# Performance work log

Hardware: AMD Instinct MI355X
Metric: run time of the kernel (lower is better)

## Reference

```python
import jax, jax.numpy as jnp
import numpy as np

DIM = 192
HEADS = 6
WS = (4, 8, 8)  # window size (D, H, W)
N = WS[0] * WS[1] * WS[2]  # 256 tokens per window
NW = 64
B_ = 256  # batch * nW


def _relative_position_index(ws):
    d, h, w = ws
    coords = jnp.stack(jnp.meshgrid(jnp.arange(d), jnp.arange(h), jnp.arange(w), indexing='ij'))
    coords = coords.reshape(3, -1)  # (3, N)
    rel = coords[:, :, None] - coords[:, None, :]  # (3, N, N)
    rel = rel.transpose(1, 2, 0) + jnp.array([d - 1, h - 1, w - 1])
    idx = rel[..., 0] * ((2 * h - 1) * (2 * w - 1)) + rel[..., 1] * (2 * w - 1) + rel[..., 2]
    return idx.astype(jnp.int32)  # (N, N)


def setup_inputs() -> dict:
    key = jax.random.key(0)
    ks = jax.random.split(key, 7)
    table_rows = (2 * WS[0] - 1) * (2 * WS[1] - 1) * (2 * WS[2] - 1)  # 1575
    return {
        'x': jax.random.normal(ks[0], (B_, N, DIM), dtype=jnp.float32),
        'mask': jax.random.normal(ks[1], (NW, N, N), dtype=jnp.float32),
        'qkv_w': jax.random.normal(ks[2], (DIM, 3 * DIM), dtype=jnp.float32) * 0.02,
        'qkv_b': jnp.zeros((3 * DIM,), dtype=jnp.float32),
        'proj_w': jax.random.normal(ks[3], (DIM, DIM), dtype=jnp.float32) * 0.02,
        'proj_b': jnp.zeros((DIM,), dtype=jnp.float32),
        'bias_table': jax.random.normal(ks[4], (table_rows, HEADS), dtype=jnp.float32) * 0.02,
        'rel_index': _relative_position_index(WS),
    }


def reference(x, mask, qkv_w, qkv_b, proj_w, proj_b, bias_table, rel_index):
    B, Ntok, C = x.shape
    hd = C // HEADS
    scale = hd ** (-0.5)
    qkv = (x @ qkv_w + qkv_b).reshape(B, Ntok, 3, HEADS, hd)
    qkv = qkv.transpose(2, 0, 3, 1, 4)  # (3, B, H, N, hd)
    q, k, v = qkv[0], qkv[1], qkv[2]
    attn = jnp.einsum('bhnd,bhmd->bhnm', q * scale, k)  # (B, H, N, N)
    # gathered relative-position bias: (N, N, H) -> (H, N, N)
    bias = bias_table[rel_index.reshape(-1)].reshape(Ntok, Ntok, HEADS).transpose(2, 0, 1)
    attn = attn + bias[None]
    nW = mask.shape[0]
    attn = attn.reshape(B // nW, nW, HEADS, Ntok, Ntok) + mask[None, :, None]
    attn = attn.reshape(B, HEADS, Ntok, Ntok)
    attn = jax.nn.softmax(attn, axis=-1)
    out = jnp.einsum('bhnm,bhmd->bhnd', attn, v)  # (B, H, N, hd)
    out = out.transpose(0, 2, 1, 3).reshape(B, Ntok, C)
    out = out @ proj_w + proj_b
    return out
```

## Files before the change

### kernel.cpp

```cpp
#include <hip/hip_runtime.h>
#include <cstdint>
#include <math.h>

#define DIMC 192
#define NTOK 256
#define HEADS 6
#define HD 32
#define L2E 1.4426950408889634f

typedef __bf16 bf16x8 __attribute__((ext_vector_type(8)));
typedef __bf16 bf16x4 __attribute__((ext_vector_type(4)));
typedef float f32x4 __attribute__((ext_vector_type(4)));

__device__ __forceinline__ void gload_lds16(const __bf16* g, __bf16* l) {
    __builtin_amdgcn_global_load_lds((const __attribute__((address_space(1))) void*)g,
                                     (__attribute__((address_space(3))) void*)l, 16, 0, 0);
}

__global__ void prep(const float* __restrict__ x, __bf16* __restrict__ xb,
                     const float* __restrict__ qkv_w, __bf16* __restrict__ wqt,
                     const float* __restrict__ proj_w, __bf16* __restrict__ wpt,
                     const float* __restrict__ table, const int* __restrict__ rel,
                     __bf16* __restrict__ biasb) {
    const int bid = blockIdx.x, t = threadIdx.x;
    if (bid < 6144) {
        int i = bid * 256 + t;
        float4 a = ((const float4*)x)[i * 2];
        float4 b = ((const float4*)x)[i * 2 + 1];
        bf16x8 o = {(__bf16)a.x, (__bf16)a.y, (__bf16)a.z, (__bf16)a.w,
                    (__bf16)b.x, (__bf16)b.y, (__bf16)b.z, (__bf16)b.w};
        ((bf16x8*)xb)[i] = o;
    } else if (bid < 6576) {
        int i = (bid - 6144) * 256 + t;
        int n = i / DIMC, k = i - n * DIMC;
        wqt[i] = (__bf16)qkv_w[(size_t)k * 576 + n];
    } else if (bid < 6720) {
        int i = (bid - 6576) * 256 + t;
        int n = i / DIMC, k = i - n * DIMC;
        wpt[i] = (__bf16)proj_w[(size_t)k * DIMC + n];
    } else {
        int i = (bid - 6720) * 256 + t;
        int h = i >> 16;
        int r = i & 65535;
        biasb[i] = (__bf16)(table[rel[r] * 6 + h] * L2E);
    }
}

__launch_bounds__(256, 2)
__global__ void qkvbm(const __bf16* __restrict__ A, const __bf16* __restrict__ Wt,
                      const float* __restrict__ bias,
                      __bf16* __restrict__ qo, __bf16* __restrict__ ko, __bf16* __restrict__ vo,
                      const float* __restrict__ mask, const __bf16* __restrict__ biasb,
                      __bf16* __restrict__ bm) {
    __shared__ __bf16 As[256 * 64];
    __shared__ __bf16 Bs[96 * 64];
    const int t = threadIdx.x;
    const int lin = blockIdx.x;

    if (lin >= 1536) {
        int i = (lin - 1536) * 256 + t;
        int w = i >> 13, oct = i & 8191;
        float4 m0 = ((const float4*)mask)[(size_t)w * 16384 + oct * 2];
        float4 m1 = ((const float4*)mask)[(size_t)w * 16384 + oct * 2 + 1];
        #pragma unroll
        for (int h = 0; h < 6; ++h) {
            bf16x8 bb = ((const bf16x8*)biasb)[h * 8192 + oct];
            bf16x8 o = {(__bf16)(m0.x * L2E + (float)bb[0]), (__bf16)(m0.y * L2E + (float)bb[1]),
                        (__bf16)(m0.z * L2E + (float)bb[2]), (__bf16)(m0.w * L2E + (float)bb[3]),
                        (__bf16)(m1.x * L2E + (float)bb[4]), (__bf16)(m1.y * L2E + (float)bb[5]),
                        (__bf16)(m1.z * L2E + (float)bb[6]), (__bf16)(m1.w * L2E + (float)bb[7])};
            ((bf16x8*)bm)[(size_t)(w * 6 + h) * 8192 + oct] = o;
        }
        return;
    }

    const int wv = t >> 6, lane = t & 63;
    const int l16 = lane & 15, quad = lane >> 4;
    const int xcd = lin & 7, pos = lin >> 3;
    const int bx = pos % 6;
    const int by = xcd + (pos / 6) * 8;
    const int m0 = by * 256;
    const int j0 = bx * 96;

    f32x4 acc[4][6];
    #pragma unroll
    for (int mt = 0; mt < 4; ++mt)
        #pragma unroll
        for (int nt = 0; nt < 6; ++nt)
            acc[mt][nt] = (f32x4){0.f, 0.f, 0.f, 0.f};

    for (int kit = 0; kit < 3; ++kit) {
        const int k0 = kit * 64;
        #pragma unroll
        for (int gi = 0; gi < 8; ++gi) {
            int g = wv * 8 + gi;
            int cid = g * 64 + lane;
            int row = cid >> 3, kcs = cid & 7;
            int kcg = kcs ^ (row & 7);
            gload_lds16(A + (size_t)(m0 + row) * DIMC + k0 + kcg * 8, As + g * 512);
        }
        #pragma unroll
        for (int gi = 0; gi < 3; ++gi) {
            int g = wv * 3 + gi;
            int cid = g * 64 + lane;
            int n = cid >> 3, kcs = cid & 7;
            int kcg = kcs ^ (n & 7);
            gload_lds16(Wt + (size_t)(j0 + n) * DIMC + k0 + kcg * 8, Bs + g * 512);
        }
        __syncthreads();
        #pragma unroll
        for (int kk = 0; kk < 2; ++kk) {
            bf16x8 af[4], bfr[6];
            #pragma unroll
            for (int mt = 0; mt < 4; ++mt) {
                int row = wv * 64 + mt * 16 + l16;
                int ch = (kk * 4 + quad) ^ (row & 7);
                af[mt] = *(const bf16x8*)(As + row * 64 + ch * 8);
            }
            #pragma unroll
            for (int nt = 0; nt < 6; ++nt) {
                int n = nt * 16 + l16;
                int ch = (kk * 4 + quad) ^ (n & 7);
                bfr[nt] = *(const bf16x8*)(Bs + n * 64 + ch * 8);
            }
            #pragma unroll
            for (int mt = 0; mt < 4; ++mt)
                #pragma unroll
                for (int nt = 0; nt < 6; ++nt)
                    acc[mt][nt] = __builtin_amdgcn_mfma_f32_16x16x32_bf16(af[mt], bfr[nt], acc[mt][nt], 0, 0, 0);
        }
        __syncthreads();
    }

    const int which = bx >> 1;
    __bf16* outp = which == 0 ? qo : (which == 1 ? ko : vo);
    const float sc = which == 0 ? (0.17677669529663687f * L2E) : 1.0f;
    float bq[6];
    #pragma unroll
    for (int nt = 0; nt < 6; ++nt) bq[nt] = bias[j0 + nt * 16 + l16];
    const int cloc = (bx & 1) * 96;
    const int b = m0 >> 8;

    if (which != 2) {
        __bf16* tile = As + wv * 4096;
        const int TP = 104;
        #pragma unroll
        for (int mt = 0; mt < 4; ++mt) {
            #pragma unroll
            for (int nt = 0; nt < 6; ++nt)
                #pragma unroll
                for (int r = 0; r < 4; ++r)
                    tile[(quad * 4 + r) * TP + nt * 16 + l16] = (__bf16)((acc[mt][nt][r] + bq[nt]) * sc);
            int row = lane >> 2;
            #pragma unroll
            for (int it = 0; it < 3; ++it) {
                int c8 = (lane & 3) + it * 4;
                bf16x8 val = *(const bf16x8*)(tile + row * TP + c8 * 8);
                int n = wv * 64 + mt * 16 + row;
                int cw = cloc + c8 * 8;
                int h = cw >> 5, d0 = cw & 31;
                *(bf16x8*)(outp + (((size_t)b * HEADS + h) * NTOK + n) * HD + d0) = val;
            }
        }
    } else {
        __bf16* tileT = As + wv * 4096;
        #pragma unroll
        for (int mt = 0; mt < 4; ++mt) {
            #pragma unroll
            for (int nt = 0; nt < 6; ++nt)
                #pragma unroll
                for (int r = 0; r < 4; ++r)
                    tileT[(nt * 16 + l16) * 16 + quad * 4 + r] = (__bf16)(acc[mt][nt][r] + bq[nt]);
            int n0 = wv * 64 + mt * 16;
            #pragma unroll
            for (int it = 0; it < 3; ++it) {
                int qid = lane + 64 * it;
                int col = qid >> 1, half = qid & 1;
                bf16x8 val = *(const bf16x8*)(tileT + col * 16 + half * 8);
                int cw = cloc + col;
                int h = cw >> 5, d = cw & 31;
                *(bf16x8*)(outp + (((size_t)b * HEADS + h) * HD + d) * NTOK + n0 + half * 8) = val;
            }
        }
    }
}

__launch_bounds__(256, 4)
__global__ void attn_mfma(const __bf16* __restrict__ qg, const __bf16* __restrict__ kg,
                          const __bf16* __restrict__ vtg, const __bf16* __restrict__ bm,
                          __bf16* __restrict__ aout) {
    __shared__ __bf16 Ps[4][16][40];
    __shared__ float  Sums[4][64];

    const int lin = blockIdx.x;
    const int xcd = lin & 7, pos = lin >> 3;
    const int g = xcd + (pos >> 2) * 8;
    const int i4 = pos & 3;
    const int h = g % 6, w = g / 6;
    const int b = i4 * 64 + w;
    const int bh = b * HEADS + h;

    const int t = threadIdx.x;
    const int wv = t >> 6, lane = t & 63;
    const int l16 = lane & 15, quad = lane >> 4;
    const int q0 = wv * 64;
    const size_t base = (size_t)bh * (NTOK * HD);

    bf16x8 qf[4];
    #pragma unroll
    for (int qt = 0; qt < 4; ++qt)
        qf[qt] = *(const bf16x8*)(qg + base + (size_t)(q0 + qt * 16 + l16) * HD + quad * 8);

    f32x4 o[4][2];
    #pragma unroll
    for (int qt = 0; qt < 4; ++qt)
        #pragma unroll
        for (int dt = 0; dt < 2; ++dt)
            o[qt][dt] = (f32x4){0.f, 0.f, 0.f, 0.f};
    float rsum[4] = {};

    const __bf16* kp  = kg  + base + (size_t)l16 * HD + quad * 8;
    const __bf16* vp  = vtg + base + (size_t)l16 * NTOK + quad * 8;
    const __bf16* bmq = bm + (size_t)(w * 6 + h) * 65536 + (size_t)(q0 + l16) * 256 + quad * 4;

    bf16x8 kf[2];
    kf[0] = *(const bf16x8*)(kp);
    kf[1] = *(const bf16x8*)(kp + 16 * HD);

    for (int c = 0; c < 8; ++c) {
        const int kb = c * 32;
        bf16x4 bmv[4][2];
        #pragma unroll
        for (int qt = 0; qt < 4; ++qt)
            #pragma unroll
            for (int kt = 0; kt < 2; ++kt)
                bmv[qt][kt] = *(const bf16x4*)(bmq + qt * 4096 + kb + kt * 16);
        bf16x8 vf[2];
        #pragma unroll
        for (int dt = 0; dt < 2; ++dt)
            vf[dt] = *(const bf16x8*)(vp + dt * 16 * NTOK + kb);
        bf16x8 kfn[2];
        if (c < 7) {
            kfn[0] = *(const bf16x8*)(kp + (kb + 32) * HD);
            kfn[1] = *(const bf16x8*)(kp + (kb + 48) * HD);
        }

        #pragma unroll
        for (int qt = 0; qt < 4; ++qt) {
            #pragma unroll
            for (int kt = 0; kt < 2; ++kt) {
                f32x4 s = (f32x4){0.f, 0.f, 0.f, 0.f};
                s = __builtin_amdgcn_mfma_f32_16x16x32_bf16(kf[kt], qf[qt], s, 0, 0, 0);
                bf16x4 pk;
                #pragma unroll
                for (int r = 0; r < 4; ++r) {
                    float p = __builtin_amdgcn_exp2f(s[r] + (float)bmv[qt][kt][r]);
                    rsum[qt] += p;
                    pk[r] = (__bf16)p;
                }
                *(bf16x4*)(&Ps[wv][l16][kt * 16 + quad * 4]) = pk;
            }
            bf16x8 pf = *(const bf16x8*)(&Ps[wv][l16][quad * 8]);
            #pragma unroll
            for (int dt = 0; dt < 2; ++dt)
                o[qt][dt] = __builtin_amdgcn_mfma_f32_16x16x32_bf16(pf, vf[dt], o[qt][dt], 0, 0, 0);
        }
        if (c < 7) { kf[0] = kfn[0]; kf[1] = kfn[1]; }
    }

    #pragma unroll
    for (int qt = 0; qt < 4; ++qt) {
        float s = rsum[qt];
        s += __shfl_xor(s, 16);
        s += __shfl_xor(s, 32);
        if (quad == 0) Sums[wv][qt * 16 + l16] = 1.0f / s;
    }
    #pragma unroll
    for (int qt = 0; qt < 4; ++qt) {
        f32x4 inv = *(const f32x4*)(&Sums[wv][qt * 16 + quad * 4]);
        #pragma unroll
        for (int dt = 0; dt < 2; ++dt)
            #pragma unroll
            for (int r = 0; r < 4; ++r) {
                int qrow = q0 + qt * 16 + quad * 4 + r;
                aout[((size_t)b * NTOK + qrow) * DIMC + h * HD + dt * 16 + l16] =
                    (__bf16)(o[qt][dt][r] * inv[r]);
            }
    }
}

__launch_bounds__(256, 2)
__global__ void proj_mfma(const __bf16* __restrict__ A, const __bf16* __restrict__ Wt,
                          const float* __restrict__ bias, float* __restrict__ out) {
    __shared__ __bf16 As[256 * 64];
    __shared__ __bf16 Bs[96 * 64];
    const int t = threadIdx.x;
    const int wv = t >> 6, lane = t & 63;
    const int l16 = lane & 15, quad = lane >> 4;

    const int lin = blockIdx.x + blockIdx.y * 2;
    const int xcd = lin & 7, pos = lin >> 3;
    const int bx = pos & 1;
    const int by = xcd + (pos >> 1) * 8;

    const int m0 = by * 256;
    const int j0 = bx * 96;

    f32x4 acc[4][6];
    #pragma unroll
    for (int mt = 0; mt < 4; ++mt)
        #pragma unroll
        for (int nt = 0; nt < 6; ++nt)
            acc[mt][nt] = (f32x4){0.f, 0.f, 0.f, 0.f};

    for (int kit = 0; kit < 3; ++kit) {
        const int k0 = kit * 64;
        #pragma unroll
        for (int gi = 0; gi < 8; ++gi) {
            int g = wv * 8 + gi;
            int cid = g * 64 + lane;
            int row = cid >> 3, kcs = cid & 7;
            int kcg = kcs ^ (row & 7);
            gload_lds16(A + (size_t)(m0 + row) * DIMC + k0 + kcg * 8, As + g * 512);
        }
        #pragma unroll
        for (int gi = 0; gi < 3; ++gi) {
            int g = wv * 3 + gi;
            int cid = g * 64 + lane;
            int n = cid >> 3, kcs = cid & 7;
            int kcg = kcs ^ (n & 7);
            gload_lds16(Wt + (size_t)(j0 + n) * DIMC + k0 + kcg * 8, Bs + g * 512);
        }
        __syncthreads();
        #pragma unroll
        for (int kk = 0; kk < 2; ++kk) {
            bf16x8 af[4], bfr[6];
            #pragma unroll
            for (int mt = 0; mt < 4; ++mt) {
                int row = wv * 64 + mt * 16 + l16;
                int ch = (kk * 4 + quad) ^ (row & 7);
                af[mt] = *(const bf16x8*)(As + row * 64 + ch * 8);
            }
            #pragma unroll
            for (int nt = 0; nt < 6; ++nt) {
                int n = nt * 16 + l16;
                int ch = (kk * 4 + quad) ^ (n & 7);
                bfr[nt] = *(const bf16x8*)(Bs + n * 64 + ch * 8);
            }
            #pragma unroll
            for (int mt = 0; mt < 4; ++mt)
                #pragma unroll
                for (int nt = 0; nt < 6; ++nt)
                    acc[mt][nt] = __builtin_amdgcn_mfma_f32_16x16x32_bf16(af[mt], bfr[nt], acc[mt][nt], 0, 0, 0);
        }
        __syncthreads();
    }

    #pragma unroll
    for (int nt = 0; nt < 6; ++nt) {
        int colg = j0 + nt * 16 + l16;
        float bv = bias[colg];
        #pragma unroll
        for (int mt = 0; mt < 4; ++mt)
            #pragma unroll
            for (int r = 0; r < 4; ++r) {
                int token = m0 + wv * 64 + mt * 16 + quad * 4 + r;
                out[(size_t)token * DIMC + colg] = acc[mt][nt][r] + bv;
            }
    }
}

extern "C" void kernel_launch(void* const* d_in, const int* in_sizes, int n_in,
                              void* d_out, int out_size, void* d_ws, size_t ws_size,
                              hipStream_t stream) {
    const float* x          = (const float*)d_in[0];
    const float* mask       = (const float*)d_in[1];
    const float* qkv_w      = (const float*)d_in[2];
    const float* qkv_b      = (const float*)d_in[3];
    const float* proj_w     = (const float*)d_in[4];
    const float* proj_b     = (const float*)d_in[5];
    const float* bias_table = (const float*)d_in[6];
    const int*   rel_index  = (const int*)d_in[7];

    char* ws = (char*)d_ws;
    __bf16* xb    = (__bf16*)(ws);
    __bf16* q     = (__bf16*)(ws + 25165824);
    __bf16* k     = (__bf16*)(ws + 50331648);
    __bf16* vT    = (__bf16*)(ws + 75497472);
    __bf16* biasb = (__bf16*)(ws + 100663296);
    __bf16* wqt   = (__bf16*)(ws + 102236160);
    __bf16* wpt   = (__bf16*)(ws + 102457344);
    __bf16* aoutb = xb;
    __bf16* bm    = (__bf16*)d_out;

    prep<<<8256, 256, 0, stream>>>(x, xb, qkv_w, wqt, proj_w, wpt, bias_table, rel_index, biasb);
    qkvbm<<<3584, 256, 0, stream>>>(xb, wqt, qkv_b, q, k, vT, mask, biasb, bm);
    attn_mfma<<<1536, 256, 0, stream>>>(q, k, vT, bm, aoutb);
    proj_mfma<<<dim3(2, 256), 256, 0, stream>>>(aoutb, wpt, proj_b, (float*)d_out);
}
```

Before: 233.2 us.

## Stage K and V^T tiles in swizzled LDS and prefetch the bias-mask one chunk ahead

The attention kernel now copies the whole K and V^T tiles for its (batch, head) pair into LDS with global_load_lds. An XOR swizzle is applied to avoid bank conflicts, and the MFMA operands are then read from LDS. Previously each of the four waves loaded them separately from global memory. The bias-plus-mask loads are double-buffered one chunk ahead, and the final normalisation broadcasts row sums with shuffles instead of an LDS scratch array. The cost is 32KB of extra LDS per block, which may lower occupancy, plus a block-wide barrier before compute begins.

```diff
diff --git a/kernel.cpp b/kernel.cpp
--- a/kernel.cpp
+++ b/kernel.cpp
@@ -189,8 +189,9 @@
 __global__ void attn_mfma(const __bf16* __restrict__ qg, const __bf16* __restrict__ kg,
                           const __bf16* __restrict__ vtg, const __bf16* __restrict__ bm,
                           __bf16* __restrict__ aout) {
+    __shared__ __bf16 Ks[NTOK * 32];
+    __shared__ __bf16 VTs[HD * 256];
     __shared__ __bf16 Ps[4][16][40];
-    __shared__ float  Sums[4][64];
 
     const int lin = blockIdx.x;
     const int xcd = lin & 7, pos = lin >> 3;
@@ -206,6 +207,24 @@
     const int q0 = wv * 64;
     const size_t base = (size_t)bh * (NTOK * HD);
 
+    #pragma unroll
+    for (int it = 0; it < 4; ++it) {
+        int grp = it * 4 + wv;
+        int cid = grp * 64 + lane;
+        int row = cid >> 2, cc = cid & 3;
+        int scc = cc ^ ((row >> 1) & 3);
+        gload_lds16(kg + base + row * HD + scc * 8, Ks + grp * 512);
+    }
+    #pragma unroll
+    for (int it = 0; it < 4; ++it) {
+        int grp = it * 4 + wv;
+        int cid = grp * 64 + lane;
+        int row = cid >> 5, cc = cid & 31;
+        int scc = cc ^ (row & 7);
+        gload_lds16(vtg + base + row * NTOK + scc * 8, VTs + grp * 512);
+    }
+    __syncthreads();
+
     bf16x8 qf[4];
     #pragma unroll
     for (int qt = 0; qt < 4; ++qt)
@@ -219,30 +238,36 @@
             o[qt][dt] = (f32x4){0.f, 0.f, 0.f, 0.f};
     float rsum[4] = {};
 
-    const __bf16* kp  = kg  + base + (size_t)l16 * HD + quad * 8;
-    const __bf16* vp  = vtg + base + (size_t)l16 * NTOK + quad * 8;
     const __bf16* bmq = bm + (size_t)(w * 6 + h) * 65536 + (size_t)(q0 + l16) * 256 + quad * 4;
-
-    bf16x8 kf[2];
-    kf[0] = *(const bf16x8*)(kp);
-    kf[1] = *(const bf16x8*)(kp + 16 * HD);
+    const int ck = quad ^ ((l16 >> 1) & 3);
+    const int xv = l16 & 7;
+
+    bf16x4 bmv[4][2];
+    #pragma unroll
+    for (int qt = 0; qt < 4; ++qt)
+        #pragma unroll
+        for (int kt = 0; kt < 2; ++kt)
+            bmv[qt][kt] = *(const bf16x4*)(bmq + qt * 4096 + kt * 16);
 
     for (int c = 0; c < 8; ++c) {
         const int kb = c * 32;
-        bf16x4 bmv[4][2];
-        #pragma unroll
-        for (int qt = 0; qt < 4; ++qt)
-            #pragma unroll
-            for (int kt = 0; kt < 2; ++kt)
-                bmv[qt][kt] = *(const bf16x4*)(bmq + qt * 4096 + kb + kt * 16);
+        bf16x4 bmn[4][2];
+        if (c < 7) {
+            #pragma unroll
+            for (int qt = 0; qt < 4; ++qt)
+                #pragma unroll
+                for (int kt = 0; kt < 2; ++kt)
+                    bmn[qt][kt] = *(const bf16x4*)(bmq + qt * 4096 + kb + 32 + kt * 16);
+        }
+        bf16x8 kf[2];
+        #pragma unroll
+        for (int kt = 0; kt < 2; ++kt)
+            kf[kt] = *(const bf16x8*)(Ks + (kb + kt * 16 + l16) * 32 + ck * 8);
         bf16x8 vf[2];
         #pragma unroll
-        for (int dt = 0; dt < 2; ++dt)
-            vf[dt] = *(const bf16x8*)(vp + dt * 16 * NTOK + kb);
-        bf16x8 kfn[2];
-        if (c < 7) {
-            kfn[0] = *(const bf16x8*)(kp + (kb + 32) * HD);
-            kfn[1] = *(const bf16x8*)(kp + (kb + 48) * HD);
+        for (int dt = 0; dt < 2; ++dt) {
+            int cv = (c * 4 + quad) ^ xv;
+            vf[dt] = *(const bf16x8*)(VTs + (dt * 16 + l16) * 256 + cv * 8);
         }
 
         #pragma unroll
@@ -265,27 +290,34 @@
             for (int dt = 0; dt < 2; ++dt)
                 o[qt][dt] = __builtin_amdgcn_mfma_f32_16x16x32_bf16(pf, vf[dt], o[qt][dt], 0, 0, 0);
         }
-        if (c < 7) { kf[0] = kfn[0]; kf[1] = kfn[1]; }
-    }
-
+        if (c < 7) {
+            #pragma unroll
+            for (int qt = 0; qt < 4; ++qt)
+                #pragma unroll
+                for (int kt = 0; kt < 2; ++kt)
+                    bmv[qt][kt] = bmn[qt][kt];
+        }
+    }
+
+    float rstot[4];
     #pragma unroll
     for (int qt = 0; qt < 4; ++qt) {
         float s = rsum[qt];
         s += __shfl_xor(s, 16);
         s += __shfl_xor(s, 32);
-        if (quad == 0) Sums[wv][qt * 16 + l16] = 1.0f / s;
+        rstot[qt] = 1.0f / s;
     }
     #pragma unroll
     for (int qt = 0; qt < 4; ++qt) {
-        f32x4 inv = *(const f32x4*)(&Sums[wv][qt * 16 + quad * 4]);
-        #pragma unroll
-        for (int dt = 0; dt < 2; ++dt)
-            #pragma unroll
-            for (int r = 0; r < 4; ++r) {
-                int qrow = q0 + qt * 16 + quad * 4 + r;
+        #pragma unroll
+        for (int r = 0; r < 4; ++r) {
+            float inv = __shfl(rstot[qt], (lane & 48) | (quad * 4 + r));
+            int qrow = q0 + qt * 16 + quad * 4 + r;
+            #pragma unroll
+            for (int dt = 0; dt < 2; ++dt)
                 aout[((size_t)b * NTOK + qrow) * DIMC + h * HD + dt * 16 + l16] =
-                    (__bf16)(o[qt][dt][r] * inv[r]);
-            }
+                    (__bf16)(o[qt][dt][r] * inv);
+        }
     }
 }
 
```

Result: faster. 226.3 us (-3.0%).
